# Kernel tuning notes

Hardware: AMD Instinct MI355X
Metric: run time of the kernel (lower is better)

## Reference

```python
import jax, jax.numpy as jnp
import numpy as np

WS = 7      # window_size
NH = 8      # num_heads
ND = 5      # n_degree -> Np = 6


def setup_inputs() -> dict:
    key = jax.random.key(0)
    ks = jax.random.split(key, 9)
    B, Q, C, H, W = 2, 100, 256, 64, 64
    Np = ND + 1
    ws2 = WS * WS
    return {
        "x": jax.random.normal(ks[0], (B, C, H, W), dtype=jnp.float32),
        "polys": jax.random.uniform(ks[1], (B, Q, 2, Np), dtype=jnp.float32),
        "w_qkv": jax.random.normal(ks[2], (3 * C, C), dtype=jnp.float32) * 0.02,
        "b_qkv": jnp.zeros((3 * C,), dtype=jnp.float32),
        "w_proj": jax.random.normal(ks[3], (C, C), dtype=jnp.float32) * 0.02,
        "b_proj": jnp.zeros((C,), dtype=jnp.float32),
        "conv_w": jax.random.normal(ks[4], (1, ws2, 1, 1), dtype=jnp.float32) * 0.1,
        "conv_b": jnp.zeros((1,), dtype=jnp.float32),
        "pos_bias": jax.random.normal(ks[5], (ws2, 1), dtype=jnp.float32),
    }


def reference(x, polys, w_qkv, b_qkv, w_proj, b_proj, conv_w, conv_b, pos_bias):
    B, C, H, W = x.shape
    _, Q, _, Np = polys.shape  # polys: [B,Q,2,n_degree+1]
    ws = WS
    ws2 = ws * ws
    nh = NH
    hd = C // nh
    scale = hd ** -0.5

    # --- polynomial -> sample points (get_points) ---
    alpha = jnp.linspace(0.0, 1.0, Np)
    alphas = jnp.stack([alpha ** i for i in range(Np - 1, -1, -1)], axis=1)  # [Np, Np]
    points = jnp.swapaxes(polys @ alphas.T, -1, -2)  # [B,Q,Np,2]
    points = 2.0 * points - 1.0
    points = points[:, :, None, :, :]  # [B,Q,1,Np,2]

    # --- deformable window grid (faithful to torch, incl. -ws//2 floor-div) ---
    lo = (-ws) // 2   # -4 for ws=7
    hi = ws // 2      #  3
    delta_h = 2.0 * jnp.linspace(lo, hi, ws) / H
    delta_w = 2.0 * jnp.linspace(lo, hi, ws) / W
    mesh_x, mesh_y = jnp.meshgrid(delta_w, delta_h, indexing='xy')  # [ws,ws]
    mesh_x = mesh_x.reshape(-1, 1)  # [ws2,1]
    mesh_y = mesh_y.reshape(-1, 1)
    grid_y = points[..., 0] + mesh_y  # [B,Q,ws2,Np]
    grid_x = points[..., 1] + mesh_x
    grid = jnp.stack((grid_y, grid_x), axis=-1)        # [B,Q,ws2,Np,2]
    grid = grid.reshape(B, Q * Np * ws2, 2)            # same flat order as torch .view

    # --- grid_sample: bilinear, zeros padding, align_corners=True ---
    # grid[...,0] -> x coordinate (width), grid[...,1] -> y (height)
    def sample_one(img, g):  # img [C,H,W], g [P,2] -> [C,P]
        fx = (g[:, 0] + 1.0) * 0.5 * (W - 1)
        fy = (g[:, 1] + 1.0) * 0.5 * (H - 1)
        x0 = jnp.floor(fx)
        y0 = jnp.floor(fy)
        wx1 = fx - x0
        wy1 = fy - y0

        def gather(yy, xx):
            valid = (xx >= 0) & (xx <= W - 1) & (yy >= 0) & (yy <= H - 1)
            xi = jnp.clip(xx, 0, W - 1).astype(jnp.int32)
            yi = jnp.clip(yy, 0, H - 1).astype(jnp.int32)
            return img[:, yi, xi] * valid.astype(img.dtype)  # [C,P]

        v00 = gather(y0, x0)
        v01 = gather(y0, x0 + 1)
        v10 = gather(y0 + 1, x0)
        v11 = gather(y0 + 1, x0 + 1)
        return (v00 * (1 - wy1) * (1 - wx1) + v01 * (1 - wy1) * wx1 +
                v10 * wy1 * (1 - wx1) + v11 * wy1 * wx1)

    sampled = jax.vmap(sample_one)(x, grid)            # [B, C, Q*Np*ws2]
    sampled = sampled.reshape(B, C, Q * Np, ws2)
    sampled = jnp.transpose(sampled, (0, 2, 1, 3))     # [B, Q*Np, C, ws2]
    sp = sampled.reshape(B, Q, Np, C, ws2)
    sp = jnp.transpose(sp, (0, 1, 2, 4, 3)).reshape(B, Q * Np, ws2, C)

    # --- windowed multi-head self-attention over each sampled patch ---
    qkv = sp @ w_qkv.T + b_qkv                          # [B,QN,ws2,3C]
    qkv = qkv.reshape(B, Q * Np, ws2, 3, nh, hd)
    qkv = jnp.transpose(qkv, (3, 0, 4, 1, 2, 5))        # [3,B,nh,QN,ws2,hd]
    q, k, v = qkv[0], qkv[1], qkv[2]
    attn = jnp.einsum('bhnpd,bhnqd->bhnpq', q, k) * scale
    attn = attn + pos_bias.reshape(1, 1, 1, ws2, 1)     # bias per query row (as in torch)
    attn = jax.nn.softmax(attn, axis=-1)
    o = jnp.einsum('bhnpq,bhnqd->bhnpd', attn, v)       # [B,nh,QN,ws2,hd]
    o = jnp.swapaxes(o, 2, 3)                           # [B,nh,ws2,QN,hd]
    o = o.reshape(B, Q * Np, ws2, C)                    # faithful torch .reshape
    o = jnp.swapaxes(o, 1, 2)                           # [B,ws2,QN,C]

    # --- conv1x1 over the ws2 channel axis, then output projection ---
    y = jnp.einsum('bwnc,w->bnc', o, conv_w.reshape(ws2)) + conv_b.reshape(1, 1, 1)
    y = y @ w_proj.T + b_proj                           # [B,QN,C]
    return y.reshape(B, Q, Np, C)
```

## Files before the change

### kernel.cpp

```cpp
#include <hip/hip_runtime.h>
#include <hip/hip_bf16.h>

#define B_    2
#define QN    100
#define NP    6
#define WS2   49
#define CC    256
#define NHH   8
#define HDD   32
#define NWIN  600
#define O_PER_B 7526400

#define XT_BYTES   (8388608 + 1024)
#define ZABS       2097152
#define WB_BYTES   393216
#define QKV_SHORTS_PER_WIN (WS2 * 768)
#define QKV_BYTES  (1200 * WS2 * 768 * 2)

#define SPB_LD 264
#define CW_LD  72

typedef __attribute__((ext_vector_type(8))) short bf16x8;
typedef __attribute__((ext_vector_type(4))) float f32x4;

__device__ __forceinline__ unsigned short f2bf(float f) {
  union { float f; unsigned int i; } v; v.f = f;
  unsigned int x = v.i;
  x += 0x7fffu + ((x >> 16) & 1u);
  return (unsigned short)(x >> 16);
}

__global__ void k0_prep(const float* __restrict__ x, float* __restrict__ xT,
                        const float* __restrict__ w_qkv, unsigned short* __restrict__ wbp) {
  __shared__ float tile[32][33];
  const int gb = blockIdx.x;
  if (gb < 2048) {
    int b   = gb >> 10;
    int rem = gb & 1023;
    int hw0 = (rem & 127) * 32;
    int c0  = (rem >> 7) * 32;
    int tx = threadIdx.x & 31, ty = threadIdx.x >> 5;
    const float* src = x + (size_t)b * CC * 4096;
    float* dst = xT + (size_t)b * 4096 * CC;
    #pragma unroll
    for (int i = ty; i < 32; i += 8)
      tile[i][tx] = src[(size_t)(c0 + i) * 4096 + hw0 + tx];
    __syncthreads();
    #pragma unroll
    for (int i = ty; i < 32; i += 8)
      dst[(size_t)(hw0 + i) * CC + c0 + tx] = tile[tx][i];
  } else if (gb < 2144) {
    int g = (gb - 2048) * 256 + threadIdx.x;
    int lane = g & 63;
    int ks = (g >> 6) & 7;
    int nt = g >> 9;
    int n  = nt * 16 + (lane & 15);
    int k0 = ks * 32 + (lane >> 4) * 8;
    const float* src = w_qkv + (size_t)n * CC + k0;
    float4 lo = *(const float4*)(src);
    float4 hi = *(const float4*)(src + 4);
    unsigned short o[8] = { f2bf(lo.x), f2bf(lo.y), f2bf(lo.z), f2bf(lo.w),
                            f2bf(hi.x), f2bf(hi.y), f2bf(hi.z), f2bf(hi.w) };
    *(uint4*)(wbp + (size_t)g * 8) = *(uint4*)o;
  } else {
    xT[ZABS + threadIdx.x] = 0.0f;
  }
}

__launch_bounds__(256, 3)
__global__ void k1_sample_qkv(const float* __restrict__ xT,
                              const float* __restrict__ polys,
                              const unsigned short* __restrict__ wbp,
                              const float* __restrict__ b_qkv,
                              unsigned short* __restrict__ qkv_ws) {
  __shared__ __align__(16) unsigned short spb[64 * SPB_LD];
  __shared__ __align__(16) unsigned short Cwbuf[4][16 * CW_LD];
  __shared__ __align__(16) int   co_off[WS2][4];
  __shared__ __align__(16) float co_w[WS2][4];
  const int tid = threadIdx.x;
  const int m = blockIdx.x;
  const int b = blockIdx.y;

  if (tid < WS2) {
    int n = m * WS2 + tid;
    int q = n / (WS2 * NP);
    int p = (n / NP) % WS2;
    int a = n % NP;
    const float* pc = polys + (size_t)(b * QN + q) * 12;
    float al = (float)a * 0.2f;
    float py = pc[0];
    float px = pc[6];
    #pragma unroll
    for (int i = 1; i < 6; i++) { py = py * al + pc[i]; px = px * al + pc[6 + i]; }
    py = 2.0f * py - 1.0f;
    px = 2.0f * px - 1.0f;
    float gy = py + (2.0f * (-4.0f + (float)(p / 7) * (7.0f / 6.0f))) * (1.0f / 64.0f);
    float gx = px + (2.0f * (-4.0f + (float)(p % 7) * (7.0f / 6.0f))) * (1.0f / 64.0f);
    float fx = (gy + 1.0f) * 0.5f * 63.0f;
    float fy = (gx + 1.0f) * 0.5f * 63.0f;
    float x0 = floorf(fx), y0 = floorf(fy);
    float wx = fx - x0, wy = fy - y0;
    float x1 = x0 + 1.0f, y1 = y0 + 1.0f;
    int xi0 = (int)fminf(fmaxf(x0, 0.0f), 63.0f);
    int yi0 = (int)fminf(fmaxf(y0, 0.0f), 63.0f);
    int xi1 = (int)fminf(fmaxf(x1, 0.0f), 63.0f);
    int yi1 = (int)fminf(fmaxf(y1, 0.0f), 63.0f);
    bool vx0 = (x0 >= 0.0f) && (x0 <= 63.0f);
    bool vx1 = (x1 >= 0.0f) && (x1 <= 63.0f);
    bool vy0 = (y0 >= 0.0f) && (y0 <= 63.0f);
    bool vy1 = (y1 >= 0.0f) && (y1 <= 63.0f);
    const int bb = b * 4096;
    co_off[tid][0] = (vx0 && vy0) ? (bb + yi0 * 64 + xi0) * CC : ZABS;
    co_off[tid][1] = (vx1 && vy0) ? (bb + yi0 * 64 + xi1) * CC : ZABS;
    co_off[tid][2] = (vx0 && vy1) ? (bb + yi1 * 64 + xi0) * CC : ZABS;
    co_off[tid][3] = (vx1 && vy1) ? (bb + yi1 * 64 + xi1) * CC : ZABS;
    co_w[tid][0] = (1.0f - wy) * (1.0f - wx);
    co_w[tid][1] = (1.0f - wy) * wx;
    co_w[tid][2] = wy * (1.0f - wx);
    co_w[tid][3] = wy * wx;
  }
  {
    unsigned int* z = (unsigned int*)(spb + WS2 * SPB_LD);
    for (int i = tid; i < 15 * SPB_LD / 2; i += 256) z[i] = 0u;
  }
  __syncthreads();

  for (int bi = 0; bi < 12; bi++) {
    const int rbase = bi * 4;
    float vv[4][4];
    #pragma unroll
    for (int k = 0; k < 4; k++) {
      int r = rbase + k;
      int4 off = *(const int4*)&co_off[r][0];
      vv[k][0] = xT[off.x + tid];
      vv[k][1] = xT[off.y + tid];
      vv[k][2] = xT[off.z + tid];
      vv[k][3] = xT[off.w + tid];
    }
    #pragma unroll
    for (int k = 0; k < 4; k++) {
      int r = rbase + k;
      float4 w = *(const float4*)&co_w[r][0];
      float s = vv[k][0] * w.x + vv[k][1] * w.y + vv[k][2] * w.z + vv[k][3] * w.w;
      spb[r * SPB_LD + tid] = f2bf(s);
    }
  }
  {
    int4 off = *(const int4*)&co_off[48][0];
    float4 w = *(const float4*)&co_w[48][0];
    float s = xT[off.x + tid] * w.x + xT[off.y + tid] * w.y
            + xT[off.z + tid] * w.z + xT[off.w + tid] * w.w;
    spb[48 * SPB_LD + tid] = f2bf(s);
  }
  __syncthreads();

  const int lane = tid & 63;
  const int wv = tid >> 6;
  const int lm = lane & 15;
  const int lg = lane >> 4;
  unsigned short* qd = qkv_ws + (size_t)(b * NWIN + m) * QKV_SHORTS_PER_WIN;
  unsigned short* Cw = &Cwbuf[wv][0];

  for (int jc = 0; jc < 3; jc++) {
    const int nt0 = wv * 12 + jc * 4;
    const int ncol0 = nt0 * 16 + lm;
    f32x4 acc[4][4];
    #pragma unroll
    for (int j4 = 0; j4 < 4; j4++) {
      float bias = b_qkv[ncol0 + j4 * 16];
      #pragma unroll
      for (int mt = 0; mt < 4; mt++) acc[mt][j4] = (f32x4){bias, bias, bias, bias};
    }
    bf16x8 bnx[4];
    #pragma unroll
    for (int j4 = 0; j4 < 4; j4++)
      bnx[j4] = *(const bf16x8*)(wbp + (size_t)(((nt0 + j4) * 8 + 0) * 64 + lane) * 8);
    #pragma unroll
    for (int ks = 0; ks < 8; ks++) {
      bf16x8 bc[4];
      #pragma unroll
      for (int j4 = 0; j4 < 4; j4++) bc[j4] = bnx[j4];
      if (ks < 7) {
        #pragma unroll
        for (int j4 = 0; j4 < 4; j4++)
          bnx[j4] = *(const bf16x8*)(wbp + (size_t)(((nt0 + j4) * 8 + ks + 1) * 64 + lane) * 8);
      }
      bf16x8 af[4];
      #pragma unroll
      for (int mt = 0; mt < 4; mt++)
        af[mt] = *(const bf16x8*)(spb + (mt * 16 + lm) * SPB_LD + ks * 32 + lg * 8);
      #pragma unroll
      for (int j4 = 0; j4 < 4; j4++)
        #pragma unroll
        for (int mt = 0; mt < 4; mt++)
          acc[mt][j4] = __builtin_amdgcn_mfma_f32_16x16x32_bf16(af[mt], bc[j4], acc[mt][j4], 0, 0, 0);
    }
    const int cbase = nt0 * 16;
    #pragma unroll
    for (int mt = 0; mt < 4; mt++) {
      #pragma unroll
      for (int reg = 0; reg < 4; reg++) {
        int rr = lg * 4 + reg;
        #pragma unroll
        for (int j4 = 0; j4 < 4; j4++)
          Cw[rr * CW_LD + j4 * 16 + lm] = f2bf(acc[mt][j4][reg]);
      }
      int r0 = mt * 16;
      #pragma unroll
      for (int half = 0; half < 2; half++) {
        int idx = half * 64 + lane;
        int r16 = idx >> 3;
        int seg = idx & 7;
        int r = r0 + r16;
        if (r < WS2)
          *(uint4*)(qd + (size_t)r * 768 + cbase + seg * 8) =
              *(const uint4*)(Cw + r16 * CW_LD + seg * 8);
      }
    }
  }
}

#define P_LD 72
#define V_LD 72
#define OW_LD 36
#define P_WAVE (WS2 * P_LD)
#define V_OFF  (4 * P_WAVE)
#define V_WAVE (32 * V_LD)

__device__ __forceinline__ void attn_head(
    const bf16x8 qf[4], const bf16x8 kf[4],
    unsigned short* P, unsigned short* Vt, float* Ow, float* ob,
    int lane, int lm, int lg) {
  const float scale = 0.17677669529663687f;
  f32x4 s[4][4];
  #pragma unroll
  for (int mt = 0; mt < 4; mt++)
    #pragma unroll
    for (int nt = 0; nt < 4; nt++) {
      s[mt][nt] = (f32x4){0.f, 0.f, 0.f, 0.f};
      s[mt][nt] = __builtin_amdgcn_mfma_f32_16x16x32_bf16(qf[mt], kf[nt], s[mt][nt], 0, 0, 0);
    }
  #pragma unroll
  for (int mt = 0; mt < 4; mt++)
    #pragma unroll
    for (int nt = 0; nt < 4; nt++) {
      bool badcol = (nt == 3) && (lm > 0);
      #pragma unroll
      for (int reg = 0; reg < 4; reg++)
        s[mt][nt][reg] = badcol ? -1e30f : s[mt][nt][reg] * scale;
    }
  #pragma unroll
  for (int mt = 0; mt < 4; mt++) {
    #pragma unroll
    for (int reg = 0; reg < 4; reg++) {
      float mx = fmaxf(fmaxf(s[mt][0][reg], s[mt][1][reg]),
                       fmaxf(s[mt][2][reg], s[mt][3][reg]));
      #pragma unroll
      for (int off = 1; off < 16; off <<= 1) mx = fmaxf(mx, __shfl_xor(mx, off));
      float sum = 0.0f;
      #pragma unroll
      for (int nt = 0; nt < 4; nt++) {
        float e = __expf(s[mt][nt][reg] - mx);
        s[mt][nt][reg] = e;
        sum += e;
      }
      #pragma unroll
      for (int off = 1; off < 16; off <<= 1) sum += __shfl_xor(sum, off);
      float inv = 1.0f / sum;
      #pragma unroll
      for (int nt = 0; nt < 4; nt++) s[mt][nt][reg] *= inv;
    }
  }
  #pragma unroll
  for (int mt = 0; mt < 4; mt++)
    #pragma unroll
    for (int nt = 0; nt < 4; nt++)
      #pragma unroll
      for (int reg = 0; reg < 4; reg++) {
        int p = mt * 16 + lg * 4 + reg;
        if (p < WS2) P[p * P_LD + nt * 16 + lm] = f2bf(s[mt][nt][reg]);
      }
  f32x4 o[4][2];
  #pragma unroll
  for (int mt = 0; mt < 4; mt++)
    #pragma unroll
    for (int nt2 = 0; nt2 < 2; nt2++) o[mt][nt2] = (f32x4){0.f, 0.f, 0.f, 0.f};
  #pragma unroll
  for (int ks = 0; ks < 2; ks++) {
    bf16x8 vf[2];
    #pragma unroll
    for (int nt2 = 0; nt2 < 2; nt2++)
      vf[nt2] = *(const bf16x8*)(Vt + (nt2 * 16 + lm) * V_LD + ks * 32 + lg * 8);
    #pragma unroll
    for (int mt = 0; mt < 4; mt++) {
      bf16x8 af = *(const bf16x8*)(P + (mt * 16 + lm) * P_LD + ks * 32 + lg * 8);
      #pragma unroll
      for (int nt2 = 0; nt2 < 2; nt2++)
        o[mt][nt2] = __builtin_amdgcn_mfma_f32_16x16x32_bf16(af, vf[nt2], o[mt][nt2], 0, 0, 0);
    }
  }
  #pragma unroll
  for (int mt = 0; mt < 4; mt++)
    #pragma unroll
    for (int reg = 0; reg < 4; reg++) {
      int p = mt * 16 + lg * 4 + reg;
      if (p < WS2) {
        #pragma unroll
        for (int nt2 = 0; nt2 < 2; nt2++)
          Ow[p * OW_LD + nt2 * 16 + lm] = o[mt][nt2][reg];
      }
    }
  for (int idx = lane; idx < WS2 * 8; idx += 64) {
    int p = idx >> 3, seg = idx & 7;
    *(uint4*)(ob + (size_t)p * (NWIN * HDD) + seg * 4) =
        *(const uint4*)(Ow + p * OW_LD + seg * 4);
  }
}

__launch_bounds__(256, 3)
__global__ void k2_attn(const unsigned short* __restrict__ qkv_ws,
                        float* __restrict__ o_ws) {
  __shared__ __align__(16) unsigned short lds[V_OFF + 4 * V_WAVE];
  const int tid = threadIdx.x;
  const int lane = tid & 63;
  const int wv = tid >> 6;
  const int lm = lane & 15;
  const int lg = lane >> 4;
  const int m = blockIdx.x;
  const int b = blockIdx.y;
  const unsigned short* wsrc = qkv_ws + (size_t)(b * NWIN + m) * QKV_SHORTS_PER_WIN;
  unsigned short* P  = lds + wv * P_WAVE;
  unsigned short* Vt = lds + V_OFF + wv * V_WAVE;
  float* Ow = (float*)P;

  {
    unsigned int* vz = (unsigned int*)Vt;
    #pragma unroll
    for (int i = 0; i < 18; i++) vz[i * 64 + lane] = 0u;
  }

  const int h0 = 2 * wv, h1 = 2 * wv + 1;
  const int vr = lane >> 2;
  const int vd0 = (lane & 3) * 8;
  uint4 vbuf[4];
  #pragma unroll
  for (int i = 0; i < 4; i++) {
    int r = vr + i * 16;
    int rc = (r > 48) ? 48 : r;
    vbuf[i] = *(const uint4*)(wsrc + (size_t)rc * 768 + 512 + h0 * HDD + vd0);
  }
  bf16x8 qf[2][4], kf[2][4];
  #pragma unroll
  for (int t = 0; t < 4; t++) {
    int r = t * 16 + lm; if (r > 48) r = 48;
    qf[0][t] = *(const bf16x8*)(wsrc + (size_t)r * 768 + h0 * HDD + lg * 8);
    kf[0][t] = *(const bf16x8*)(wsrc + (size_t)r * 768 + 256 + h0 * HDD + lg * 8);
    qf[1][t] = *(const bf16x8*)(wsrc + (size_t)r * 768 + h1 * HDD + lg * 8);
    kf[1][t] = *(const bf16x8*)(wsrc + (size_t)r * 768 + 256 + h1 * HDD + lg * 8);
  }
  #pragma unroll
  for (int i = 0; i < 4; i++) {
    int r = vr + i * 16;
    if (r < WS2) {
      unsigned int uu[4] = { vbuf[i].x, vbuf[i].y, vbuf[i].z, vbuf[i].w };
      #pragma unroll
      for (int k = 0; k < 4; k++) {
        Vt[(vd0 + 2 * k) * V_LD + r]     = (unsigned short)(uu[k] & 0xffffu);
        Vt[(vd0 + 2 * k + 1) * V_LD + r] = (unsigned short)(uu[k] >> 16);
      }
    }
  }

  float* ob0 = o_ws + (size_t)b * O_PER_B + ((size_t)h0 * WS2 * NWIN + m) * HDD;
  float* ob1 = o_ws + (size_t)b * O_PER_B + ((size_t)h1 * WS2 * NWIN + m) * HDD;

  uint4 vbuf2[4];
  #pragma unroll
  for (int i = 0; i < 4; i++) {
    int r = vr + i * 16;
    int rc = (r > 48) ? 48 : r;
    vbuf2[i] = *(const uint4*)(wsrc + (size_t)rc * 768 + 512 + h1 * HDD + vd0);
  }

  attn_head(qf[0], kf[0], P, Vt, Ow, ob0, lane, lm, lg);

  #pragma unroll
  for (int i = 0; i < 4; i++) {
    int r = vr + i * 16;
    if (r < WS2) {
      unsigned int uu[4] = { vbuf2[i].x, vbuf2[i].y, vbuf2[i].z, vbuf2[i].w };
      #pragma unroll
      for (int k = 0; k < 4; k++) {
        Vt[(vd0 + 2 * k) * V_LD + r]     = (unsigned short)(uu[k] & 0xffffu);
        Vt[(vd0 + 2 * k + 1) * V_LD + r] = (unsigned short)(uu[k] >> 16);
      }
    }
  }

  attn_head(qf[1], kf[1], P, Vt, Ow, ob1, lane, lm, lg);
}

__global__ void k3_conv_proj(const float* __restrict__ o_ws,
                             const float* __restrict__ conv_w,
                             const float* __restrict__ conv_b,
                             const float* __restrict__ w_proj,
                             const float* __restrict__ b_proj,
                             float* __restrict__ out) {
  __shared__ float yv[CC];
  __shared__ float cw[WS2];
  const int tid = threadIdx.x;
  const int np = blockIdx.x;
  const int b = blockIdx.y;
  if (tid < WS2) cw[tid] = conv_w[tid];
  __syncthreads();
  const float* base = o_ws + (size_t)b * O_PER_B + (size_t)np * (WS2 * CC);
  float acc = conv_b[0];
  for (int p = 0; p < WS2; p++)
    acc += cw[p] * base[p * CC + tid];
  yv[tid] = acc;
  __syncthreads();
  const float4* y4 = (const float4*)yv;
  const float4* w4 = (const float4*)(w_proj + (size_t)tid * CC);
  float s = b_proj[tid];
  float s2 = 0.0f;
  #pragma unroll 8
  for (int c4 = 0; c4 < 64; c4++) {
    float4 a = y4[c4], wv2 = w4[c4];
    s2 += a.x * wv2.x + a.y * wv2.y + a.z * wv2.z + a.w * wv2.w;
  }
  out[((size_t)(b * NWIN + np)) * CC + tid] = s + s2;
}

extern "C" void kernel_launch(void* const* d_in, const int* in_sizes, int n_in,
                              void* d_out, int out_size, void* d_ws, size_t ws_size,
                              hipStream_t stream) {
  const float* x        = (const float*)d_in[0];
  const float* polys    = (const float*)d_in[1];
  const float* w_qkv    = (const float*)d_in[2];
  const float* b_qkv    = (const float*)d_in[3];
  const float* w_proj   = (const float*)d_in[4];
  const float* b_proj   = (const float*)d_in[5];
  const float* conv_w   = (const float*)d_in[6];
  const float* conv_b   = (const float*)d_in[7];
  float* out = (float*)d_out;

  char* ws = (char*)d_ws;
  float* xT = (float*)ws;
  unsigned short* wbp = (unsigned short*)(ws + XT_BYTES);
  unsigned short* qkv_ws = (unsigned short*)(ws + XT_BYTES + WB_BYTES);
  float* o_ws = (float*)(ws + XT_BYTES + WB_BYTES + QKV_BYTES);

  hipLaunchKernelGGL(k0_prep, dim3(2145), dim3(256), 0, stream, x, xT, w_qkv, wbp);
  hipLaunchKernelGGL(k1_sample_qkv, dim3(NWIN, B_), dim3(256), 0, stream,
                     xT, polys, wbp, b_qkv, qkv_ws);
  hipLaunchKernelGGL(k2_attn, dim3(NWIN, B_), dim3(256), 0, stream,
                     qkv_ws, o_ws);
  hipLaunchKernelGGL(k3_conv_proj, dim3(NWIN, B_), dim3(256), 0, stream,
                     o_ws, conv_w, conv_b, w_proj, b_proj, out);
}
```

Measured before the change: 194.8 us.

## Store attention output as bf16 in contiguous per-window layout, gather via index table

The attention kernel now writes its per-head output as bf16 into a contiguous per-window, per-head block instead of scattered fp32 rows. This halves the intermediate traffic between attention and the conv/projection stage and makes the attention kernel's stores contiguous. The conv/projection kernel reconstructs the torch reshape mapping through a small LDS index table and gathers bf16 values, so its reads become less regular. It also adds bf16 rounding error on the intermediate.

```diff
diff --git a/kernel.cpp b/kernel.cpp
--- a/kernel.cpp
+++ b/kernel.cpp
@@ -28,6 +28,9 @@
   unsigned int x = v.i;
   x += 0x7fffu + ((x >> 16) & 1u);
   return (unsigned short)(x >> 16);
+}
+__device__ __forceinline__ float bf2f(unsigned short u) {
+  union { unsigned int i; float f; } v; v.i = ((unsigned int)u) << 16; return v.f;
 }
 
 __global__ void k0_prep(const float* __restrict__ x, float* __restrict__ xT,
@@ -229,7 +232,7 @@
 
 __device__ __forceinline__ void attn_head(
     const bf16x8 qf[4], const bf16x8 kf[4],
-    unsigned short* P, unsigned short* Vt, float* Ow, float* ob,
+    unsigned short* P, unsigned short* Vt, float* Ow, unsigned short* ob16,
     int lane, int lm, int lg) {
   const float scale = 0.17677669529663687f;
   f32x4 s[4][4];
@@ -310,16 +313,19 @@
           Ow[p * OW_LD + nt2 * 16 + lm] = o[mt][nt2][reg];
       }
     }
-  for (int idx = lane; idx < WS2 * 8; idx += 64) {
-    int p = idx >> 3, seg = idx & 7;
-    *(uint4*)(ob + (size_t)p * (NWIN * HDD) + seg * 4) =
-        *(const uint4*)(Ow + p * OW_LD + seg * 4);
+  for (int idx = lane; idx < WS2 * 4; idx += 64) {
+    int p = idx >> 2, seg = idx & 3;
+    const float* src = Ow + p * OW_LD + seg * 8;
+    unsigned short o8[8];
+    #pragma unroll
+    for (int k = 0; k < 8; k++) o8[k] = f2bf(src[k]);
+    *(uint4*)(ob16 + (size_t)idx * 8) = *(uint4*)o8;
   }
 }
 
 __launch_bounds__(256, 3)
 __global__ void k2_attn(const unsigned short* __restrict__ qkv_ws,
-                        float* __restrict__ o_ws) {
+                        unsigned short* __restrict__ o16) {
   __shared__ __align__(16) unsigned short lds[V_OFF + 4 * V_WAVE];
   const int tid = threadIdx.x;
   const int lane = tid & 63;
@@ -371,8 +377,9 @@
     }
   }
 
-  float* ob0 = o_ws + (size_t)b * O_PER_B + ((size_t)h0 * WS2 * NWIN + m) * HDD;
-  float* ob1 = o_ws + (size_t)b * O_PER_B + ((size_t)h1 * WS2 * NWIN + m) * HDD;
+  unsigned short* obase = o16 + ((size_t)(b * NWIN + m) * 392) * 32;
+  unsigned short* ob0 = obase + (size_t)h0 * WS2 * HDD;
+  unsigned short* ob1 = obase + (size_t)h1 * WS2 * HDD;
 
   uint4 vbuf2[4];
   #pragma unroll
@@ -400,7 +407,7 @@
   attn_head(qf[1], kf[1], P, Vt, Ow, ob1, lane, lm, lg);
 }
 
-__global__ void k3_conv_proj(const float* __restrict__ o_ws,
+__global__ void k3_conv_proj(const unsigned short* __restrict__ o16,
                              const float* __restrict__ conv_w,
                              const float* __restrict__ conv_b,
                              const float* __restrict__ w_proj,
@@ -408,15 +415,22 @@
                              float* __restrict__ out) {
   __shared__ float yv[CC];
   __shared__ float cw[WS2];
+  __shared__ int atab[392];
   const int tid = threadIdx.x;
   const int np = blockIdx.x;
   const int b = blockIdx.y;
   if (tid < WS2) cw[tid] = conv_w[tid];
+  for (int i = tid; i < 392; i += 256) {
+    int Q = np * 392 + i;
+    int m = Q % 600;
+    int hp = Q / 600;
+    atab[i] = ((b * NWIN + m) * 392 + hp) * 32;
+  }
   __syncthreads();
-  const float* base = o_ws + (size_t)b * O_PER_B + (size_t)np * (WS2 * CC);
+  const int cg = tid >> 5, dd = tid & 31;
   float acc = conv_b[0];
   for (int p = 0; p < WS2; p++)
-    acc += cw[p] * base[p * CC + tid];
+    acc += cw[p] * bf2f(o16[(size_t)atab[p * 8 + cg] + dd]);
   yv[tid] = acc;
   __syncthreads();
   const float4* y4 = (const float4*)yv;
@@ -448,13 +462,13 @@
   float* xT = (float*)ws;
   unsigned short* wbp = (unsigned short*)(ws + XT_BYTES);
   unsigned short* qkv_ws = (unsigned short*)(ws + XT_BYTES + WB_BYTES);
-  float* o_ws = (float*)(ws + XT_BYTES + WB_BYTES + QKV_BYTES);
+  unsigned short* o16 = (unsigned short*)(ws + XT_BYTES + WB_BYTES + QKV_BYTES);
 
   hipLaunchKernelGGL(k0_prep, dim3(2145), dim3(256), 0, stream, x, xT, w_qkv, wbp);
   hipLaunchKernelGGL(k1_sample_qkv, dim3(NWIN, B_), dim3(256), 0, stream,
                      xT, polys, wbp, b_qkv, qkv_ws);
   hipLaunchKernelGGL(k2_attn, dim3(NWIN, B_), dim3(256), 0, stream,
-                     qkv_ws, o_ws);
+                     qkv_ws, o16);
   hipLaunchKernelGGL(k3_conv_proj, dim3(NWIN, B_), dim3(256), 0, stream,
-                     o_ws, conv_w, conv_b, w_proj, b_proj, out);
-}
+                     o16, conv_w, conv_b, w_proj, b_proj, out);
+}
```

Result: no change. 193.7 us (-0.5%).
